# Kernel optimization log

Measured on AMD Instinct MI355X. Metric: run time of the kernel, lower is better.

## Reference

```python
import jax, jax.numpy as jnp
import numpy as np

KH = KW = 3
STRIDE = 1
PAD = 1
DIL = 1


def setup_inputs() -> dict:
    key = jax.random.key(0)
    k1, k2, k3 = jax.random.split(key, 3)
    x = jax.random.normal(k1, (4, 256, 80, 80), dtype=jnp.float32)
    offset = jax.random.normal(k2, (4, 18, 80, 80), dtype=jnp.float32)
    weight = jax.random.normal(k3, (256, 256, 3, 3), dtype=jnp.float32) * 0.05
    return {"x": x, "offset": offset, "weight": weight}


def _deform_conv(x, offset, weight):
    # Naive deformable conv: bilinear-sample each of the kh*kw kernel taps at
    # (regular grid location + learned offset), then a dense GEMM with weight.
    # Sampling uses grid_sample semantics with align_corners=True (the torch
    # code normalizes by (L-1)/2) and zeros padding -> pure pixel coordinates.
    N, C, H, W = x.shape
    oh, ow = offset.shape[2], offset.shape[3]
    kk = KH * KW
    # offset layout: (N, dg=1, kh, kw, 2, oh, ow); channel 0 = y, 1 = x
    off = offset.reshape(N, KH, KW, 2, oh, ow)
    off_y = off[:, :, :, 0].reshape(N, kk, oh, ow)
    off_x = off[:, :, :, 1].reshape(N, kk, oh, ow)

    ky, kx = jnp.meshgrid(jnp.arange(KH), jnp.arange(KW), indexing='ij')
    ky = (ky.reshape(kk) * DIL).astype(x.dtype)
    kx = (kx.reshape(kk) * DIL).astype(x.dtype)
    base_y = jnp.arange(oh, dtype=x.dtype) * STRIDE - PAD  # [oh]
    base_x = jnp.arange(ow, dtype=x.dtype) * STRIDE - PAD  # [ow]

    # absolute sampling coords, [N, kk, oh, ow]
    py = off_y + ky[None, :, None, None] + base_y[None, None, :, None]
    px = off_x + kx[None, :, None, None] + base_x[None, None, None, :]

    x0 = jnp.floor(px)
    y0 = jnp.floor(py)
    x1 = x0 + 1.0
    y1 = y0 + 1.0
    wx1 = px - x0
    wx0 = 1.0 - wx1
    wy1 = py - y0
    wy0 = 1.0 - wy1

    x_flat = x.reshape(N, C, H * W)

    def corner(xc, yc, w):
        # zeros padding: out-of-bounds corners contribute 0
        m = ((xc >= 0) & (xc <= W - 1) & (yc >= 0) & (yc <= H - 1)).astype(x.dtype)
        xi = jnp.clip(xc, 0, W - 1).astype(jnp.int32)
        yi = jnp.clip(yc, 0, H - 1).astype(jnp.int32)
        idx = yi * W + xi  # [N, kk, oh, ow]
        g = jax.vmap(lambda f, i: f[:, i])(x_flat, idx)  # [N, C, kk, oh, ow]
        return g * (w * m)[:, None]

    sampled = (corner(x0, y0, wx0 * wy0) + corner(x1, y0, wx1 * wy0)
               + corner(x0, y1, wx0 * wy1) + corner(x1, y1, wx1 * wy1))

    OC = weight.shape[0]
    # weight flattens as (oc, c, kh, kw) -> (oc, c*kk); sampled matches (c, kk)
    out = jnp.einsum('of,nfp->nop', weight.reshape(OC, C * kk),
                     sampled.reshape(N, C * kk, oh * ow))
    return out.reshape(N, OC, oh, ow)


def reference(x, offset, weight):
    return _deform_conv(x, offset, weight)
```

## Files before the change

### kernel.cpp

```cpp
#include <hip/hip_runtime.h>


typedef short short8 __attribute__((ext_vector_type(8)));
typedef float floatx4 __attribute__((ext_vector_type(4)));
typedef float floatx2 __attribute__((ext_vector_type(2)));
typedef unsigned int uint4v __attribute__((ext_vector_type(4)));

#define Cc    256
#define OCc   256
#define Hh    80
#define Ww    80
#define HW    6400
#define KK    9
#define Ktot  2304
#define PT    64
#define KC    64
#define NCHUNK (Ktot / KC)
#define NKB   (Ktot / 32)
#define WP_ELEMS (Ktot * OCc)
#define XT_OFF   ((size_t)WP_ELEMS)
#define PREP_W_BLOCKS 288

#define BARRIER_LDS()                                      \
  do {                                                     \
    asm volatile("s_waitcnt lgkmcnt(0)" ::: "memory");     \
    __builtin_amdgcn_s_barrier();                          \
  } while (0)

__device__ __forceinline__ unsigned short f2bf(float f) {
  unsigned u = __float_as_uint(f);
  u += 0x7FFF + ((u >> 16) & 1);
  return (unsigned short)(u >> 16);
}
__device__ __forceinline__ unsigned int cvtpk(float lo, float hi) {
  unsigned int r;
  asm("v_cvt_pk_bf16_f32 %0, %1, %2" : "=v"(r) : "v"(lo), "v"(hi));
  return r;
}

__global__ void prep(const float* __restrict__ w, const float* __restrict__ x,
                     unsigned short* __restrict__ wp,
                     unsigned short* __restrict__ xt) {
  __shared__ float tile[64][65];
  const int tid = threadIdx.x;
  if (blockIdx.x < PREP_W_BLOCKS) {
    const int t = blockIdx.x * 256 + tid;
    const int lane = t & 63;
    const int ocf  = (t >> 6) & 15;
    const int kb   = t >> 10;
    const int oc   = ocf * 16 + (lane & 15);
    const int k0   = kb * 32 + (lane >> 4) * 8;
    const int tap  = k0 >> 8;
    const int c0   = k0 & 255;
    const float* src = w + (size_t)oc * Ktot + (size_t)c0 * KK + tap;
    short8 pk;
    #pragma unroll
    for (int e = 0; e < 8; ++e) pk[e] = (short)f2bf(src[e * KK]);
    *(short8*)(wp + (size_t)t * 8) = pk;
    return;
  }
  const int b = blockIdx.x - PREP_W_BLOCKS;
  const int hw0 = (b % 100) * 64;
  const int c0  = ((b / 100) & 3) * 64;
  const int n   = b / 400;
  #pragma unroll
  for (int i = 0; i < 16; ++i) {
    const int idx = i * 256 + tid;
    const int cl = idx >> 6, hl = idx & 63;
    tile[cl][hl] = x[((size_t)(n * Cc + c0 + cl)) * HW + hw0 + hl];
  }
  __syncthreads();
  #pragma unroll
  for (int i = 0; i < 16; ++i) {
    const int idx = i * 256 + tid;
    const int hl = idx >> 6, cl = idx & 63;
    xt[((size_t)(n * HW + hw0 + hl)) * Cc + c0 + cl] = f2bf(tile[cl][hl]);
  }
}

__global__ __launch_bounds__(512, 4) void dcn_mfma(
    const float* __restrict__ x, const float* __restrict__ offset,
    const unsigned short* __restrict__ wp,
    const unsigned short* __restrict__ xt, float* __restrict__ out) {
  __shared__ unsigned short s_col[3][PT * KC];
  __shared__ float4 s_w[KK * PT];
  __shared__ int4   s_i[KK * PT];

  const int tid  = threadIdx.x;
  const int lane = tid & 63;
  const int wv   = tid >> 6;

  const int bid  = blockIdx.x;
  const int logical = (bid & 7) * 50 + (bid >> 3);
  const int nn   = logical / 100;
  const int tile = logical - nn * 100;
  const int p0   = tile * PT;
  const char* xn = (const char*)(xt + (size_t)nn * HW * Cc);

  for (int s = tid; s < KK * PT; s += 512) {
    const int k = s / PT, p = s % PT;
    const int pp = p0 + p;
    const int oy = pp / Ww, ox = pp % Ww;
    const int ky = k / 3, kx = k % 3;
    const float offy = offset[(size_t)(nn * 18 + 2 * k    ) * HW + pp];
    const float offx = offset[(size_t)(nn * 18 + 2 * k + 1) * HW + pp];
    const float py = offy + (float)(ky + oy - 1);
    const float px = offx + (float)(kx + ox - 1);
    const float fy0 = floorf(py), fx0 = floorf(px);
    const int iy0 = (int)fy0, ix0 = (int)fx0;
    const float wy1 = py - fy0, wx1 = px - fx0;
    const float wy0 = 1.f - wy1, wx0 = 1.f - wx1;
    const bool my0 = (iy0     >= 0) & (iy0     < Hh);
    const bool my1 = (iy0 + 1 >= 0) & (iy0 + 1 < Hh);
    const bool mx0 = (ix0     >= 0) & (ix0     < Ww);
    const bool mx1 = (ix0 + 1 >= 0) & (ix0 + 1 < Ww);
    const int cy0 = min(max(iy0,     0), Hh - 1);
    const int cy1 = min(max(iy0 + 1, 0), Hh - 1);
    const int cx0 = min(max(ix0,     0), Ww - 1);
    const int cx1 = min(max(ix0 + 1, 0), Ww - 1);
    float4 w4;
    w4.x = wx0 * wy0 * ((my0 && mx0) ? 1.f : 0.f);
    w4.y = wx1 * wy0 * ((my0 && mx1) ? 1.f : 0.f);
    w4.z = wx0 * wy1 * ((my1 && mx0) ? 1.f : 0.f);
    w4.w = wx1 * wy1 * ((my1 && mx1) ? 1.f : 0.f);
    int4 i4;
    i4.x = (cy0 * Ww + cx0) * 512;  i4.y = (cy0 * Ww + cx1) * 512;
    i4.z = (cy1 * Ww + cx0) * 512;  i4.w = (cy1 * Ww + cx1) * 512;
    s_w[s] = w4;
    s_i[s] = i4;
  }

  floatx4 acc[2][4] = {};
  const int lm = lane & 15, lg = lane >> 4;
  const int spx = tid >> 3;
  const int cg  = tid & 7;
  const int wbyte = spx * 128 + ((cg * 16) ^ ((spx & 7) << 4));
  __syncthreads();

  short8 raA, rbA, rcA, rdA, raB, rbB, rcB, rdB;
  short8 fA00, fA01, fA10, fA11, fB00, fB01, fB10, fB11;

  #define ISSUE(ch, S)                                                  \
    { const int tap_ = (ch) >> 2;                                       \
      const int coff_ = (((ch) & 3) * KC + cg * 8) * 2;                 \
      const int4 i4_ = s_i[tap_ * PT + spx];                            \
      ra##S = *(const short8*)(xn + i4_.x + coff_);                     \
      rb##S = *(const short8*)(xn + i4_.y + coff_);                     \
      rc##S = *(const short8*)(xn + i4_.z + coff_);                     \
      rd##S = *(const short8*)(xn + i4_.w + coff_); }

  #define PREFA(ch, S)                                                  \
    { const unsigned short* w0_ = wp + (size_t)((ch) * 2) * (16 * 64 * 8) \
                                     + (size_t)((wv * 2) * 64 + lane) * 8; \
      f##S##00 = *(const short8*)(w0_);                                 \
      f##S##01 = *(const short8*)(w0_ + 64 * 8);                        \
      f##S##10 = *(const short8*)(w0_ + 16 * 64 * 8);                   \
      f##S##11 = *(const short8*)(w0_ + 16 * 64 * 8 + 64 * 8); }

  #define FINISH(ch, S)                                                 \
    { const int tap_ = (ch) >> 2;                                       \
      const float4 w4_ = s_w[tap_ * PT + spx];                          \
      const uint4v ua_ = __builtin_bit_cast(uint4v, ra##S);             \
      const uint4v ub_ = __builtin_bit_cast(uint4v, rb##S);             \
      const uint4v uc_ = __builtin_bit_cast(uint4v, rc##S);             \
      const uint4v ud_ = __builtin_bit_cast(uint4v, rd##S);             \
      uint4v pk_;                                                       \
      _Pragma("unroll")                                                 \
      for (int r_ = 0; r_ < 4; ++r_) {                                  \
        floatx2 va_, vb_, vc_, vd_;                                     \
        va_[0] = __uint_as_float(ua_[r_] << 16);                        \
        va_[1] = __uint_as_float(ua_[r_] & 0xFFFF0000u);                \
        vb_[0] = __uint_as_float(ub_[r_] << 16);                        \
        vb_[1] = __uint_as_float(ub_[r_] & 0xFFFF0000u);                \
        vc_[0] = __uint_as_float(uc_[r_] << 16);                        \
        vc_[1] = __uint_as_float(uc_[r_] & 0xFFFF0000u);                \
        vd_[0] = __uint_as_float(ud_[r_] << 16);                        \
        vd_[1] = __uint_as_float(ud_[r_] & 0xFFFF0000u);                \
        const floatx2 v_ = w4_.x * va_ + w4_.y * vb_                    \
                         + w4_.z * vc_ + w4_.w * vd_;                   \
        pk_[r_] = cvtpk(v_[0], v_[1]);                                  \
      }                                                                 \
      *(uint4v*)((char*)s_col[(ch) % 3] + wbyte) = pk_; }

  #define MFMA_STEP(ch, S)                                              \
    { const char* base_ = (const char*)s_col[(ch) % 3];                 \
      __builtin_amdgcn_s_setprio(1);                                    \
      _Pragma("unroll")                                                 \
      for (int ks = 0; ks < 2; ++ks) {                                  \
        short8 b_[4];                                                   \
        _Pragma("unroll")                                               \
        for (int j = 0; j < 4; ++j) {                                   \
          const int px_ = j * 16 + lm;                                  \
          const int byte_ = px_ * 128 + (((ks * 64) + lg * 16) ^ ((px_ & 7) << 4)); \
          b_[j] = *(const short8*)(base_ + byte_);                      \
        }                                                               \
        const short8 a0_ = ks ? f##S##10 : f##S##00;                    \
        const short8 a1_ = ks ? f##S##11 : f##S##01;                    \
        _Pragma("unroll")                                               \
        for (int j = 0; j < 4; ++j)                                     \
          acc[0][j] = __builtin_amdgcn_mfma_f32_16x16x32_bf16(a0_, b_[j], acc[0][j], 0, 0, 0); \
        _Pragma("unroll")                                               \
        for (int j = 0; j < 4; ++j)                                     \
          acc[1][j] = __builtin_amdgcn_mfma_f32_16x16x32_bf16(a1_, b_[j], acc[1][j], 0, 0, 0); \
      }                                                                 \
      __builtin_amdgcn_s_setprio(0); }

  PREFA(0, A);
  ISSUE(0, A);
  FINISH(0, A);
  ISSUE(1, A);
  BARRIER_LDS();

  for (int it = 0; it < NCHUNK / 2; ++it) {
    const int ch = it * 2;
    MFMA_STEP(ch, A);
    PREFA(ch + 1, B);
    if (ch + 2 < NCHUNK) ISSUE(ch + 2, B);
    FINISH(ch + 1, A);
    BARRIER_LDS();
    MFMA_STEP(ch + 1, B);
    if (ch + 2 < NCHUNK) PREFA(ch + 2, A);
    if (ch + 3 < NCHUNK) ISSUE(ch + 3, A);
    if (ch + 2 < NCHUNK) FINISH(ch + 2, B);
    BARRIER_LDS();
  }

  #pragma unroll
  for (int f = 0; f < 2; ++f) {
    const int oc = (wv * 2 + f) * 16 + lg * 4;
    #pragma unroll
    for (int j = 0; j < 4; ++j) {
      const int px = p0 + j * 16 + lm;
      #pragma unroll
      for (int r = 0; r < 4; ++r) {
        out[(size_t)(nn * OCc + oc + r) * HW + px] = acc[f][j][r];
      }
    }
  }
}

extern "C" void kernel_launch(void* const* d_in, const int* in_sizes, int n_in,
                              void* d_out, int out_size, void* d_ws, size_t ws_size,
                              hipStream_t stream) {
  const float* x      = (const float*)d_in[0];
  const float* offset = (const float*)d_in[1];
  const float* weight = (const float*)d_in[2];
  float* out = (float*)d_out;
  unsigned short* wp = (unsigned short*)d_ws;
  unsigned short* xt = (unsigned short*)d_ws + XT_OFF;

  prep<<<dim3(PREP_W_BLOCKS + 1600), dim3(256), 0, stream>>>(weight, x, wp, xt);
  dcn_mfma<<<dim3(400), dim3(512), 0, stream>>>(x, offset, wp, xt, out);
}
```

Measured before the change: 65.39 us.

## Use 112-pixel tiles with 64-pixel tail blocks to launch exactly 256 blocks

The main kernel now has a templated body with two tile widths. Most blocks handle 112 output pixels (7 MFMA fragments), and a few tail blocks handle 64, so each image splits into 64 blocks and the grid totals 256, one per CU. The im2col LDS buffer drops from triple to double buffering, and launch bounds go from 4 waves per SIMD to 2 to leave room for the larger tiles. The aim is to cut weight refetches per pixel and remove the partial last wave of 400 blocks. The cost is uneven work between block types and more registers per thread, and the halved occupancy gives less latency hiding for the gathers.

```diff
diff --git a/kernel.cpp b/kernel.cpp
--- a/kernel.cpp
+++ b/kernel.cpp
@@ -13,10 +13,10 @@
 #define HW    6400
 #define KK    9
 #define Ktot  2304
-#define PT    64
 #define KC    64
 #define NCHUNK (Ktot / KC)
 #define NKB   (Ktot / 32)
+#define PTMAX 112
 #define WP_ELEMS (Ktot * OCc)
 #define XT_OFF   ((size_t)WP_ELEMS)
 #define PREP_W_BLOCKS 288
@@ -78,27 +78,17 @@
   }
 }
 
-__global__ __launch_bounds__(512, 4) void dcn_mfma(
-    const float* __restrict__ x, const float* __restrict__ offset,
-    const unsigned short* __restrict__ wp,
-    const unsigned short* __restrict__ xt, float* __restrict__ out) {
-  __shared__ unsigned short s_col[3][PT * KC];
-  __shared__ float4 s_w[KK * PT];
-  __shared__ int4   s_i[KK * PT];
-
-  const int tid  = threadIdx.x;
-  const int lane = tid & 63;
-  const int wv   = tid >> 6;
-
-  const int bid  = blockIdx.x;
-  const int logical = (bid & 7) * 50 + (bid >> 3);
-  const int nn   = logical / 100;
-  const int tile = logical - nn * 100;
-  const int p0   = tile * PT;
-  const char* xn = (const char*)(xt + (size_t)nn * HW * Cc);
-
-  for (int s = tid; s < KK * PT; s += 512) {
-    const int k = s / PT, p = s % PT;
+template <int NFRAG>
+__device__ __forceinline__ void dcn_body(
+    const int tid, const int lane, const int wv, const int nn, const int p0,
+    const float* __restrict__ offset, const unsigned short* __restrict__ wp,
+    const char* __restrict__ xn, float* __restrict__ out,
+    char* __restrict__ slab, float4* __restrict__ s_w, int4* __restrict__ s_i) {
+  constexpr int PTl = NFRAG * 16;
+  constexpr int SLOTS = PTl * 8;
+
+  for (int s = tid; s < KK * PTl; s += 512) {
+    const int k = s / PTl, p = s % PTl;
     const int pp = p0 + p;
     const int oy = pp / Ww, ox = pp % Ww;
     const int ky = k / 3, kx = k % 3;
@@ -130,24 +120,35 @@
     s_i[s] = i4;
   }
 
-  floatx4 acc[2][4] = {};
+  floatx4 acc[2][NFRAG] = {};
   const int lm = lane & 15, lg = lane >> 4;
-  const int spx = tid >> 3;
-  const int cg  = tid & 7;
-  const int wbyte = spx * 128 + ((cg * 16) ^ ((spx & 7) << 4));
+  const int spx1 = tid >> 3;
+  const int cg   = tid & 7;
+  const int spx2 = 64 + (tid >> 3);
+  const bool r2  = (NFRAG == 7) && (tid < (SLOTS - 512));
+  const int wbyte1 = spx1 * 128 + ((cg * 16) ^ ((spx1 & 7) << 4));
+  const int wbyte2 = spx2 * 128 + ((cg * 16) ^ ((spx2 & 7) << 4));
   __syncthreads();
 
   short8 raA, rbA, rcA, rdA, raB, rbB, rcB, rdB;
+  short8 reA, rfA, rgA, rhA, reB, rfB, rgB, rhB;
   short8 fA00, fA01, fA10, fA11, fB00, fB01, fB10, fB11;
 
   #define ISSUE(ch, S)                                                  \
     { const int tap_ = (ch) >> 2;                                       \
       const int coff_ = (((ch) & 3) * KC + cg * 8) * 2;                 \
-      const int4 i4_ = s_i[tap_ * PT + spx];                            \
-      ra##S = *(const short8*)(xn + i4_.x + coff_);                     \
-      rb##S = *(const short8*)(xn + i4_.y + coff_);                     \
-      rc##S = *(const short8*)(xn + i4_.z + coff_);                     \
-      rd##S = *(const short8*)(xn + i4_.w + coff_); }
+      const int4 i1_ = s_i[tap_ * PTl + spx1];                          \
+      ra##S = *(const short8*)(xn + i1_.x + coff_);                     \
+      rb##S = *(const short8*)(xn + i1_.y + coff_);                     \
+      rc##S = *(const short8*)(xn + i1_.z + coff_);                     \
+      rd##S = *(const short8*)(xn + i1_.w + coff_);                     \
+      if constexpr (NFRAG == 7) if (r2) {                               \
+        const int4 i2_ = s_i[tap_ * PTl + spx2];                        \
+        re##S = *(const short8*)(xn + i2_.x + coff_);                   \
+        rf##S = *(const short8*)(xn + i2_.y + coff_);                   \
+        rg##S = *(const short8*)(xn + i2_.z + coff_);                   \
+        rh##S = *(const short8*)(xn + i2_.w + coff_);                   \
+      } }
 
   #define PREFA(ch, S)                                                  \
     { const unsigned short* w0_ = wp + (size_t)((ch) * 2) * (16 * 64 * 8) \
@@ -157,14 +158,11 @@
       f##S##10 = *(const short8*)(w0_ + 16 * 64 * 8);                   \
       f##S##11 = *(const short8*)(w0_ + 16 * 64 * 8 + 64 * 8); }
 
-  #define FINISH(ch, S)                                                 \
-    { const int tap_ = (ch) >> 2;                                       \
-      const float4 w4_ = s_w[tap_ * PT + spx];                          \
-      const uint4v ua_ = __builtin_bit_cast(uint4v, ra##S);             \
-      const uint4v ub_ = __builtin_bit_cast(uint4v, rb##S);             \
-      const uint4v uc_ = __builtin_bit_cast(uint4v, rc##S);             \
-      const uint4v ud_ = __builtin_bit_cast(uint4v, rd##S);             \
-      uint4v pk_;                                                       \
+  #define COMBINE(pa, pb, pc, pd, w4_, dst_)                            \
+    { const uint4v ua_ = __builtin_bit_cast(uint4v, pa);                \
+      const uint4v ub_ = __builtin_bit_cast(uint4v, pb);                \
+      const uint4v uc_ = __builtin_bit_cast(uint4v, pc);                \
+      const uint4v ud_ = __builtin_bit_cast(uint4v, pd);                \
       _Pragma("unroll")                                                 \
       for (int r_ = 0; r_ < 4; ++r_) {                                  \
         floatx2 va_, vb_, vc_, vd_;                                     \
@@ -178,18 +176,30 @@
         vd_[1] = __uint_as_float(ud_[r_] & 0xFFFF0000u);                \
         const floatx2 v_ = w4_.x * va_ + w4_.y * vb_                    \
                          + w4_.z * vc_ + w4_.w * vd_;                   \
-        pk_[r_] = cvtpk(v_[0], v_[1]);                                  \
-      }                                                                 \
-      *(uint4v*)((char*)s_col[(ch) % 3] + wbyte) = pk_; }
+        dst_[r_] = cvtpk(v_[0], v_[1]);                                 \
+      } }
+
+  #define FINISH(ch, S)                                                 \
+    { const int tap_ = (ch) >> 2;                                       \
+      char* buf_ = slab + ((ch) & 1) * (PTl * 128);                     \
+      { const float4 w4_ = s_w[tap_ * PTl + spx1];                      \
+        uint4v pk_;                                                     \
+        COMBINE(ra##S, rb##S, rc##S, rd##S, w4_, pk_);                  \
+        *(uint4v*)(buf_ + wbyte1) = pk_; }                              \
+      if constexpr (NFRAG == 7) if (r2) {                               \
+        const float4 w4_ = s_w[tap_ * PTl + spx2];                      \
+        uint4v pk_;                                                     \
+        COMBINE(re##S, rf##S, rg##S, rh##S, w4_, pk_);                  \
+        *(uint4v*)(buf_ + wbyte2) = pk_; } }
 
   #define MFMA_STEP(ch, S)                                              \
-    { const char* base_ = (const char*)s_col[(ch) % 3];                 \
+    { const char* base_ = slab + ((ch) & 1) * (PTl * 128);              \
       __builtin_amdgcn_s_setprio(1);                                    \
       _Pragma("unroll")                                                 \
       for (int ks = 0; ks < 2; ++ks) {                                  \
-        short8 b_[4];                                                   \
+        short8 b_[NFRAG];                                               \
         _Pragma("unroll")                                               \
-        for (int j = 0; j < 4; ++j) {                                   \
+        for (int j = 0; j < NFRAG; ++j) {                               \
           const int px_ = j * 16 + lm;                                  \
           const int byte_ = px_ * 128 + (((ks * 64) + lg * 16) ^ ((px_ & 7) << 4)); \
           b_[j] = *(const short8*)(base_ + byte_);                      \
@@ -197,10 +207,10 @@
         const short8 a0_ = ks ? f##S##10 : f##S##00;                    \
         const short8 a1_ = ks ? f##S##11 : f##S##01;                    \
         _Pragma("unroll")                                               \
-        for (int j = 0; j < 4; ++j)                                     \
+        for (int j = 0; j < NFRAG; ++j)                                 \
           acc[0][j] = __builtin_amdgcn_mfma_f32_16x16x32_bf16(a0_, b_[j], acc[0][j], 0, 0, 0); \
         _Pragma("unroll")                                               \
-        for (int j = 0; j < 4; ++j)                                     \
+        for (int j = 0; j < NFRAG; ++j)                                 \
           acc[1][j] = __builtin_amdgcn_mfma_f32_16x16x32_bf16(a1_, b_[j], acc[1][j], 0, 0, 0); \
       }                                                                 \
       __builtin_amdgcn_s_setprio(0); }
@@ -229,13 +239,44 @@
   for (int f = 0; f < 2; ++f) {
     const int oc = (wv * 2 + f) * 16 + lg * 4;
     #pragma unroll
-    for (int j = 0; j < 4; ++j) {
+    for (int j = 0; j < NFRAG; ++j) {
       const int px = p0 + j * 16 + lm;
       #pragma unroll
       for (int r = 0; r < 4; ++r) {
         out[(size_t)(nn * OCc + oc + r) * HW + px] = acc[f][j][r];
       }
     }
+  }
+  #undef ISSUE
+  #undef PREFA
+  #undef COMBINE
+  #undef FINISH
+  #undef MFMA_STEP
+}
+
+__global__ __launch_bounds__(512, 2) void dcn_mfma(
+    const float* __restrict__ offset, const unsigned short* __restrict__ wp,
+    const unsigned short* __restrict__ xt, float* __restrict__ out) {
+  __shared__ unsigned short s_col[2][PTMAX * KC];
+  __shared__ float4 s_w[KK * PTMAX];
+  __shared__ int4   s_i[KK * PTMAX];
+
+  const int tid  = threadIdx.x;
+  const int lane = tid & 63;
+  const int wv   = tid >> 6;
+
+  const int bid = blockIdx.x;
+  const int logical = (bid & 7) * 32 + (bid >> 3);
+  const int nn = logical >> 6;
+  const int b  = logical & 63;
+  const char* xn = (const char*)(xt + (size_t)nn * HW * Cc);
+
+  if (b < 48) {
+    dcn_body<7>(tid, lane, wv, nn, b * 112, offset, wp, xn, out,
+                (char*)s_col, s_w, s_i);
+  } else {
+    dcn_body<4>(tid, lane, wv, nn, 5376 + (b - 48) * 64, offset, wp, xn, out,
+                (char*)s_col, s_w, s_i);
   }
 }
 
@@ -250,5 +291,5 @@
   unsigned short* xt = (unsigned short*)d_ws + XT_OFF;
 
   prep<<<dim3(PREP_W_BLOCKS + 1600), dim3(256), 0, stream>>>(weight, x, wp, xt);
-  dcn_mfma<<<dim3(400), dim3(512), 0, stream>>>(x, offset, wp, xt, out);
-}
+  dcn_mfma<<<dim3(256), dim3(512), 0, stream>>>(offset, wp, xt, out);
+}
```

Result: slower. 67.94 us (+3.9%).

## Split fused deformable conv into separate sampling and GEMM kernels via im2col buffer

Applied to the files above, without the earlier changes.

Adds a dedicated sampling kernel that performs bilinear interpolation over all taps and channels and writes a bf16 swizzled column buffer to workspace. A separate GEMM kernel then streams that buffer into LDS with global_load_lds and runs MFMA against prepacked weights. This drops the in-loop gather and interpolation from the GEMM pipeline, at the cost of writing and re-reading roughly 118 MB of column data and one extra launch. The fused path is kept as a fallback when workspace is too small.

```diff
diff --git a/kernel.cpp b/kernel.cpp
--- a/kernel.cpp
+++ b/kernel.cpp
@@ -19,6 +19,9 @@
 #define NKB   (Ktot / 32)
 #define WP_ELEMS (Ktot * OCc)
 #define XT_OFF   ((size_t)WP_ELEMS)
+#define COL_OFF  (XT_OFF + (size_t)4 * HW * Cc)
+#define IMG_COL_ELEMS ((size_t)HW * Ktot)
+#define SPLIT_WS_BYTES ((COL_OFF + 4 * IMG_COL_ELEMS) * 2)
 #define PREP_W_BLOCKS 288
 
 #define BARRIER_LDS()                                      \
@@ -78,6 +81,168 @@
   }
 }
 
+
+__global__ __launch_bounds__(256) void dcn_sample(
+    const float* __restrict__ offset, const unsigned short* __restrict__ xt,
+    unsigned short* __restrict__ col) {
+  const int bid = blockIdx.x;
+  const int logical = (bid & 7) * 100 + (bid >> 3);
+  const int nn = logical / 200;
+  const int sb = logical % 200;
+  const int slot = sb * 256 + threadIdx.x;
+  const int px = slot >> 3;
+  const int cg = slot & 7;
+  const int t  = px >> 6;
+  const int pl = px & 63;
+  const int oy = px / Ww, ox = px - oy * Ww;
+  const char* xn = (const char*)(xt + (size_t)nn * HW * Cc);
+  char* cb = (char*)(col + (size_t)nn * IMG_COL_ELEMS)
+           + (size_t)t * (64 * Ktot * 2) + pl * 128 + cg * 16;
+
+  for (int tap = 0; tap < KK; ++tap) {
+    const int ky = tap / 3, kx = tap - ky * 3;
+    const float offy = offset[(size_t)(nn * 18 + 2 * tap    ) * HW + px];
+    const float offx = offset[(size_t)(nn * 18 + 2 * tap + 1) * HW + px];
+    const float py  = offy + (float)(ky + oy - 1);
+    const float pxc = offx + (float)(kx + ox - 1);
+    const float fy0 = floorf(py), fx0 = floorf(pxc);
+    const int iy0 = (int)fy0, ix0 = (int)fx0;
+    const float wy1 = py - fy0, wx1 = pxc - fx0;
+    const float wy0 = 1.f - wy1, wx0 = 1.f - wx1;
+    const bool my0 = (iy0     >= 0) & (iy0     < Hh);
+    const bool my1 = (iy0 + 1 >= 0) & (iy0 + 1 < Hh);
+    const bool mx0 = (ix0     >= 0) & (ix0     < Ww);
+    const bool mx1 = (ix0 + 1 >= 0) & (ix0 + 1 < Ww);
+    const int cy0 = min(max(iy0,     0), Hh - 1);
+    const int cy1 = min(max(iy0 + 1, 0), Hh - 1);
+    const int cx0 = min(max(ix0,     0), Ww - 1);
+    const int cx1 = min(max(ix0 + 1, 0), Ww - 1);
+    float4 w4;
+    w4.x = wx0 * wy0 * ((my0 && mx0) ? 1.f : 0.f);
+    w4.y = wx1 * wy0 * ((my0 && mx1) ? 1.f : 0.f);
+    w4.z = wx0 * wy1 * ((my1 && mx0) ? 1.f : 0.f);
+    w4.w = wx1 * wy1 * ((my1 && mx1) ? 1.f : 0.f);
+    const int ia = (cy0 * Ww + cx0) * 512, ib = (cy0 * Ww + cx1) * 512;
+    const int ic = (cy1 * Ww + cx0) * 512, id = (cy1 * Ww + cx1) * 512;
+    #pragma unroll
+    for (int c4 = 0; c4 < 4; ++c4) {
+      const int coff = (c4 * KC + cg * 8) * 2;
+      const short8 ra = *(const short8*)(xn + ia + coff);
+      const short8 rb = *(const short8*)(xn + ib + coff);
+      const short8 rc = *(const short8*)(xn + ic + coff);
+      const short8 rd = *(const short8*)(xn + id + coff);
+      const uint4v ua = __builtin_bit_cast(uint4v, ra);
+      const uint4v ub = __builtin_bit_cast(uint4v, rb);
+      const uint4v uc = __builtin_bit_cast(uint4v, rc);
+      const uint4v ud = __builtin_bit_cast(uint4v, rd);
+      uint4v pk;
+      #pragma unroll
+      for (int r = 0; r < 4; ++r) {
+        floatx2 va, vb, vc, vd;
+        va[0] = __uint_as_float(ua[r] << 16);
+        va[1] = __uint_as_float(ua[r] & 0xFFFF0000u);
+        vb[0] = __uint_as_float(ub[r] << 16);
+        vb[1] = __uint_as_float(ub[r] & 0xFFFF0000u);
+        vc[0] = __uint_as_float(uc[r] << 16);
+        vc[1] = __uint_as_float(uc[r] & 0xFFFF0000u);
+        vd[0] = __uint_as_float(ud[r] << 16);
+        vd[1] = __uint_as_float(ud[r] & 0xFFFF0000u);
+        const floatx2 v = w4.x * va + w4.y * vb + w4.z * vc + w4.w * vd;
+        pk[r] = cvtpk(v[0], v[1]);
+      }
+      *(uint4v*)(cb + (size_t)(tap * 4 + c4) * 8192) = pk;
+    }
+  }
+}
+
+__global__ __launch_bounds__(512, 4) void dcn_gemm(
+    const unsigned short* __restrict__ wp,
+    const unsigned short* __restrict__ col, float* __restrict__ out) {
+  __shared__ unsigned short s_b[2][PT * KC];
+
+  const int tid = threadIdx.x, lane = tid & 63, wv = tid >> 6;
+  const int bid = blockIdx.x;
+  const int logical = (bid & 7) * 50 + (bid >> 3);
+  const int nn = logical / 100, t = logical % 100;
+  const int p0 = t * PT;
+  const int lm = lane & 15, lg = lane >> 4;
+
+  const int spx = tid >> 3, sk = tid & 7;
+  const char* src0 = (const char*)(col + (size_t)nn * IMG_COL_ELEMS)
+      + (size_t)t * (64 * Ktot * 2) + spx * 128
+      + ((sk * 16) ^ ((spx & 7) << 4));
+
+  floatx4 acc[2][4] = {};
+  short8 fA00, fA01, fA10, fA11, fB00, fB01, fB10, fB11;
+
+  #define GSTAGE(ch, buf)                                               \
+    __builtin_amdgcn_global_load_lds(                                   \
+        (const unsigned int*)(src0 + (size_t)(ch) * 8192),              \
+        (unsigned int*)(&s_b[buf][0] + wv * 512), 16, 0, 0);
+
+  #define GPREFA(ch, S)                                                 \
+    { const unsigned short* w0_ = wp + (size_t)((ch) * 2) * (16 * 64 * 8) \
+                                     + (size_t)((wv * 2) * 64 + lane) * 8; \
+      f##S##00 = *(const short8*)(w0_);                                 \
+      f##S##01 = *(const short8*)(w0_ + 64 * 8);                        \
+      f##S##10 = *(const short8*)(w0_ + 16 * 64 * 8);                   \
+      f##S##11 = *(const short8*)(w0_ + 16 * 64 * 8 + 64 * 8); }
+
+  #define GMFMA(S, buf)                                                 \
+    { const char* base_ = (const char*)s_b[buf];                        \
+      __builtin_amdgcn_s_setprio(1);                                    \
+      _Pragma("unroll")                                                 \
+      for (int ks = 0; ks < 2; ++ks) {                                  \
+        short8 b_[4];                                                   \
+        _Pragma("unroll")                                               \
+        for (int j = 0; j < 4; ++j) {                                   \
+          const int px_ = j * 16 + lm;                                  \
+          const int byte_ = px_ * 128 + (((ks * 64) + lg * 16) ^ ((px_ & 7) << 4)); \
+          b_[j] = *(const short8*)(base_ + byte_);                      \
+        }                                                               \
+        const short8 a0_ = ks ? f##S##10 : f##S##00;                    \
+        const short8 a1_ = ks ? f##S##11 : f##S##01;                    \
+        _Pragma("unroll")                                               \
+        for (int j = 0; j < 4; ++j)                                     \
+          acc[0][j] = __builtin_amdgcn_mfma_f32_16x16x32_bf16(a0_, b_[j], acc[0][j], 0, 0, 0); \
+        _Pragma("unroll")                                               \
+        for (int j = 0; j < 4; ++j)                                     \
+          acc[1][j] = __builtin_amdgcn_mfma_f32_16x16x32_bf16(a1_, b_[j], acc[1][j], 0, 0, 0); \
+      }                                                                 \
+      __builtin_amdgcn_s_setprio(0); }
+
+  GPREFA(0, A);
+  GSTAGE(0, 0);
+  __syncthreads();
+
+  for (int it = 0; it < NCHUNK / 2; ++it) {
+    const int ch = it * 2;
+    GSTAGE(ch + 1, 1);
+    GPREFA(ch + 1, B);
+    GMFMA(A, 0);
+    __syncthreads();
+    if (ch + 2 < NCHUNK) { GSTAGE(ch + 2, 0); GPREFA(ch + 2, A); }
+    GMFMA(B, 1);
+    __syncthreads();
+  }
+
+  #pragma unroll
+  for (int f = 0; f < 2; ++f) {
+    const int oc = (wv * 2 + f) * 16 + lg * 4;
+    #pragma unroll
+    for (int j = 0; j < 4; ++j) {
+      const int px = p0 + j * 16 + lm;
+      #pragma unroll
+      for (int r = 0; r < 4; ++r) {
+        out[(size_t)(nn * OCc + oc + r) * HW + px] = acc[f][j][r];
+      }
+    }
+  }
+  #undef GSTAGE
+  #undef GPREFA
+  #undef GMFMA
+}
+
 __global__ __launch_bounds__(512, 4) void dcn_mfma(
     const float* __restrict__ x, const float* __restrict__ offset,
     const unsigned short* __restrict__ wp,
@@ -89,7 +254,6 @@
   const int tid  = threadIdx.x;
   const int lane = tid & 63;
   const int wv   = tid >> 6;
-
   const int bid  = blockIdx.x;
   const int logical = (bid & 7) * 50 + (bid >> 3);
   const int nn   = logical / 100;
@@ -237,6 +401,10 @@
       }
     }
   }
+  #undef ISSUE
+  #undef PREFA
+  #undef FINISH
+  #undef MFMA_STEP
 }
 
 extern "C" void kernel_launch(void* const* d_in, const int* in_sizes, int n_in,
@@ -250,5 +418,12 @@
   unsigned short* xt = (unsigned short*)d_ws + XT_OFF;
 
   prep<<<dim3(PREP_W_BLOCKS + 1600), dim3(256), 0, stream>>>(weight, x, wp, xt);
-  dcn_mfma<<<dim3(400), dim3(512), 0, stream>>>(x, offset, wp, xt, out);
-}
+
+  if (ws_size >= (size_t)SPLIT_WS_BYTES) {
+    unsigned short* colp = (unsigned short*)d_ws + COL_OFF;
+    dcn_sample<<<dim3(800), dim3(256), 0, stream>>>(offset, xt, colp);
+    dcn_gemm<<<dim3(400), dim3(512), 0, stream>>>(wp, colp, out);
+  } else {
+    dcn_mfma<<<dim3(400), dim3(512), 0, stream>>>(x, offset, wp, xt, out);
+  }
+}
```

After: 77.26 us. +18.2%, slower.
